# Optimization experiments

Hardware: AMD Instinct MI355X
Metric: run time of the kernel (lower is better)

The kernel has to match this reference:

```python
import jax, jax.numpy as jnp
import numpy as np

D = 1024
H = 16
DH = D // H  # 64


def setup_inputs() -> dict:
    key = jax.random.key(0)
    ks = jax.random.split(key, 11)
    B, S = 2, 2048
    s = 1.0 / np.sqrt(D)  # torch Linear default init scale (uniform bound)
    mk = lambda k, shape: jax.random.uniform(k, shape, jnp.float32, -s, s)
    return {
        "q": jax.random.normal(ks[0], (B, S, D), jnp.float32),
        "k": jax.random.normal(ks[1], (B, S, D), jnp.float32),
        "v": jax.random.normal(ks[2], (B, S, D), jnp.float32),
        "Wq": mk(ks[3], (D, D)), "bq": mk(ks[4], (D,)),
        "Wk": mk(ks[5], (D, D)), "bk": mk(ks[6], (D,)),
        "Wv": mk(ks[7], (D, D)), "bv": mk(ks[8], (D,)),
        "Wo": mk(ks[9], (D, D)), "bo": mk(ks[10], (D,)),
    }


def reference(q, k, v, Wq, bq, Wk, bk, Wv, bv, Wo, bo):
    B, S, _ = q.shape
    scaling = DH ** (-0.5)
    # torch Linear: x @ W.T + b ; then split heads -> (B, H, S, DH)
    split = lambda x: x.reshape(B, -1, H, DH).transpose(0, 2, 1, 3)
    Q = split(q @ Wq.T + bq)
    K = split(k @ Wk.T + bk)
    V = split(v @ Wv.T + bv)
    scores = jnp.einsum("bhqd,bhkd->bhqk", Q, K) * scaling  # [B,H,S,S]
    attn = jax.nn.softmax(scores, axis=-1)
    out = jnp.einsum("bhqk,bhkd->bhqd", attn, V)
    out = out.transpose(0, 2, 1, 3).reshape(B, S, D)
    return out @ Wo.T + bo
```

## Files before the change

kernel.cpp:

```cpp
#include <hip/hip_runtime.h>
#include <stdint.h>

#define DIM   1024
#define HEADS 16
#define DHEAD 64
#define SEQ   2048
#define MROWS 4096
#define NQ    (MROWS * DIM)
#define NW    (DIM * DIM)

typedef unsigned short u16;
typedef __attribute__((ext_vector_type(8))) short short8;
typedef __attribute__((ext_vector_type(4))) float f32x4;
typedef __attribute__((ext_vector_type(16))) float f32x16;

static_assert(sizeof(short8) == 16, "short8 must be 16B");

__device__ __forceinline__ float bf2f(u16 u) {
  union { float f; uint32_t u; } x; x.u = ((uint32_t)u) << 16; return x.f;
}
__device__ __forceinline__ u16 f2bf(float f) {
  union { float f; uint32_t u; } x; x.f = f;
  uint32_t r = x.u + 0x7FFFu + ((x.u >> 16) & 1u);
  return (u16)(r >> 16);
}
__device__ __forceinline__ float asf(uint32_t u) {
  union { float f; uint32_t u; } x; x.u = u; return x.f;
}
__device__ __forceinline__ uint32_t cvtpk(float lo, float hi) {
  uint32_t r;
  asm("v_cvt_pk_bf16_f32 %0, %1, %2" : "=v"(r) : "v"(lo), "v"(hi));
  return r;
}
__device__ __forceinline__ float exp2fast(float x) {
#if __has_builtin(__builtin_amdgcn_exp2f)
  return __builtin_amdgcn_exp2f(x);
#else
  return __expf(x * 0.69314718055994531f);
#endif
}

#if __has_builtin(__builtin_amdgcn_global_load_lds)
#define HAVE_GLLDS 1
#else
#define HAVE_GLLDS 0
#endif

__device__ __forceinline__ void stage16(const u16* src, u16* ldsbase, int cb, int lane) {
#if HAVE_GLLDS
  (void)lane;
  __builtin_amdgcn_global_load_lds((const __attribute__((address_space(1))) void*)src,
                                   (__attribute__((address_space(3))) void*)(ldsbase + (size_t)cb * 8),
                                   16, 0, 0);
#else
  *(short8*)(ldsbase + ((size_t)cb + lane) * 8) = *(const short8*)src;
#endif
}

__global__ __launch_bounds__(256)
void cvt_all(const float* __restrict__ q, const float* __restrict__ k, const float* __restrict__ v,
             const float* __restrict__ wq, const float* __restrict__ wk,
             const float* __restrict__ wv, const float* __restrict__ wo,
             u16* __restrict__ qc, u16* __restrict__ kc, u16* __restrict__ vc,
             u16* __restrict__ wqc, u16* __restrict__ wkc, u16* __restrict__ wvc, u16* __restrict__ woc)
{
  const float* s; u16* d; int n;
  switch (blockIdx.y) {
    case 0: s = q;  d = qc;  n = NQ; break;
    case 1: s = k;  d = kc;  n = NQ; break;
    case 2: s = v;  d = vc;  n = NQ; break;
    case 3: s = wq; d = wqc; n = NW; break;
    case 4: s = wk; d = wkc; n = NW; break;
    case 5: s = wv; d = wvc; n = NW; break;
    default: s = wo; d = woc; n = NW; break;
  }
  const int n8 = n >> 3;
  for (int i = blockIdx.x * blockDim.x + threadIdx.x; i < n8; i += gridDim.x * blockDim.x) {
    float4 f0 = ((const float4*)s)[2 * i];
    float4 f1 = ((const float4*)s)[2 * i + 1];
    union { uint32_t w[4]; short8 s8; } u;
    u.w[0] = cvtpk(f0.x, f0.y); u.w[1] = cvtpk(f0.z, f0.w);
    u.w[2] = cvtpk(f1.x, f1.y); u.w[3] = cvtpk(f1.z, f1.w);
    ((short8*)d)[i] = u.s8;
  }
}

__global__ __launch_bounds__(256)
void gemm_qkv(const u16* __restrict__ A0, const u16* __restrict__ W0, const float* __restrict__ b0, u16* __restrict__ O0, float s0_,
              const u16* __restrict__ A1, const u16* __restrict__ W1, const float* __restrict__ b1, u16* __restrict__ O1, float s1_,
              const u16* __restrict__ A2, const u16* __restrict__ W2, const float* __restrict__ b2, u16* __restrict__ O2, float s2_)
{
  constexpr int BM = 128, BN = 128, BK = 64, RM = 4, RN = 4;
  __shared__ u16 As[BM * BK];
  __shared__ u16 Bs[BN * BK];

  const u16* A = A0; const u16* W = W0; const float* bias = b0; u16* O = O0; float oscale = s0_;
  if (blockIdx.z == 1) { A = A1; W = W1; bias = b1; O = O1; oscale = s1_; }
  else if (blockIdx.z == 2) { A = A2; W = W2; bias = b2; O = O2; oscale = s2_; }

  const int tid  = threadIdx.x;
  const int wave = tid >> 6, lane = tid & 63;
  const int g = lane >> 4, cc = lane & 15;
  const int wr = wave >> 1, wc = wave & 1;
  const int m0 = blockIdx.x * BM, n0 = blockIdx.y * BN;

  f32x4 acc[RM][RN];
  for (int m = 0; m < RM; ++m)
    for (int n = 0; n < RN; ++n) acc[m][n] = (f32x4){0.f, 0.f, 0.f, 0.f};

  for (int k0 = 0; k0 < DIM; k0 += BK) {
    __syncthreads();
    constexpr int AI = (BM * 8) / 256;
    for (int i = 0; i < AI; ++i) {
      int cb = (wave * AI + i) * 64;
      int ch = cb + lane;
      int row = ch >> 3, kc = ch & 7;
      stage16(A + (size_t)(m0 + row) * DIM + k0 + kc * 8, As, cb, lane);
    }
    constexpr int BI = (BN * 8) / 256;
    for (int i = 0; i < BI; ++i) {
      int cb = (wave * BI + i) * 64;
      int ch = cb + lane;
      int row = ch >> 3, kc = ch & 7;
      stage16(W + (size_t)(n0 + row) * DIM + k0 + kc * 8, Bs, cb, lane);
    }
    __syncthreads();

    for (int kk = 0; kk < 2; ++kk) {
      short8 af[RM], bfr[RN];
      for (int m = 0; m < RM; ++m)
        af[m] = *(const short8*)(As + (size_t)(wr * 64 + m * 16 + cc) * BK + kk * 32 + g * 8);
      for (int n = 0; n < RN; ++n)
        bfr[n] = *(const short8*)(Bs + (size_t)(wc * 64 + n * 16 + cc) * BK + kk * 32 + g * 8);
      for (int m = 0; m < RM; ++m)
        for (int n = 0; n < RN; ++n)
          acc[m][n] = __builtin_amdgcn_mfma_f32_16x16x32_bf16(af[m], bfr[n], acc[m][n], 0, 0, 0);
    }
  }

  for (int n = 0; n < RN; ++n) {
    int col = n0 + wc * 64 + n * 16 + cc;
    float bv = bias[col];
    for (int m = 0; m < RM; ++m) {
      int rowb = m0 + wr * 64 + m * 16 + g * 4;
      for (int r = 0; r < 4; ++r) {
        int row = rowb + r;
        float val = (acc[m][n][r] + bv) * oscale;
        int b = row >> 11, s = row & (SEQ - 1);
        int hh = col >> 6, dh = col & 63;
        O[((((size_t)b * HEADS + hh) * SEQ + s) << 6) + dh] = f2bf(val);
      }
    }
  }
}

__global__ __launch_bounds__(256)
void gemm_out(const u16* __restrict__ Op0, const u16* __restrict__ Op1,
              const float* __restrict__ lstats, const u16* __restrict__ W,
              const float* __restrict__ bias, float* __restrict__ Out)
{
  constexpr int BM = 64, BN = 128, BK = 64, RM = 2, RN = 4;
  __shared__ u16 As[BM * BK];
  __shared__ u16 Bs[BN * BK];
  __shared__ float wtab[HEADS * BM];

  const int tid  = threadIdx.x;
  const int wave = tid >> 6, lane = tid & 63;
  const int g = lane >> 4, cc = lane & 15;
  const int wr = wave >> 1, wc = wave & 1;
  const int m0 = blockIdx.x * BM, n0 = blockIdx.y * BN;

  for (int e = tid; e < HEADS * BM; e += 256) {
    int h = e >> 6, r = e & 63;
    int row = m0 + r;
    int b = row >> 11, s = row & (SEQ - 1);
    float l0 = lstats[(size_t)(b * 16 + h) * SEQ + s];
    float l1 = lstats[(size_t)(32 + b * 16 + h) * SEQ + s];
    wtab[e] = 1.0f / (l0 + l1);
  }

  f32x4 acc[RM][RN];
  for (int m = 0; m < RM; ++m)
    for (int n = 0; n < RN; ++n) acc[m][n] = (f32x4){0.f, 0.f, 0.f, 0.f};

  for (int k0 = 0; k0 < DIM; k0 += BK) {
    __syncthreads();
    const int h = k0 >> 6;
    constexpr int AI = (BM * 8) / 256;
    #pragma unroll
    for (int i = 0; i < AI; ++i) {
      int ch = (wave * AI + i) * 64 + lane;
      int row = ch >> 3, kc = ch & 7;
      int grow = m0 + row;
      int b = grow >> 11, s = grow & (SEQ - 1);
      size_t off = ((size_t)(b * 16 + h) * SEQ + s) * 64 + kc * 8;
      short8 a8 = *(const short8*)(Op0 + off);
      short8 b8 = *(const short8*)(Op1 + off);
      float winv = wtab[h * BM + row];
      union { uint32_t w[4]; short8 s8; } u;
      const uint32_t* wa = (const uint32_t*)&a8;
      const uint32_t* wb = (const uint32_t*)&b8;
      #pragma unroll
      for (int j = 0; j < 4; ++j) {
        float lo = (asf(wa[j] << 16) + asf(wb[j] << 16)) * winv;
        float hi2 = (asf(wa[j] & 0xffff0000u) + asf(wb[j] & 0xffff0000u)) * winv;
        u.w[j] = cvtpk(lo, hi2);
      }
      *(short8*)(As + (size_t)ch * 8) = u.s8;
    }
    constexpr int BI = (BN * 8) / 256;
    for (int i = 0; i < BI; ++i) {
      int cb = (wave * BI + i) * 64;
      int ch = cb + lane;
      int row = ch >> 3, kc = ch & 7;
      stage16(W + (size_t)(n0 + row) * DIM + k0 + kc * 8, Bs, cb, lane);
    }
    __syncthreads();

    for (int kk = 0; kk < 2; ++kk) {
      short8 af[RM], bfr[RN];
      for (int m = 0; m < RM; ++m)
        af[m] = *(const short8*)(As + (size_t)(wr * 32 + m * 16 + cc) * BK + kk * 32 + g * 8);
      for (int n = 0; n < RN; ++n)
        bfr[n] = *(const short8*)(Bs + (size_t)(wc * 64 + n * 16 + cc) * BK + kk * 32 + g * 8);
      for (int m = 0; m < RM; ++m)
        for (int n = 0; n < RN; ++n)
          acc[m][n] = __builtin_amdgcn_mfma_f32_16x16x32_bf16(af[m], bfr[n], acc[m][n], 0, 0, 0);
    }
  }

  for (int n = 0; n < RN; ++n) {
    int col = n0 + wc * 64 + n * 16 + cc;
    float bv = bias[col];
    for (int m = 0; m < RM; ++m) {
      int rowb = m0 + wr * 32 + m * 16 + g * 4;
      for (int r = 0; r < 4; ++r)
        Out[(size_t)(rowb + r) * DIM + col] = acc[m][n][r] + bv;
    }
  }
}

#if __has_builtin(__builtin_amdgcn_permlane32_swap)
typedef __attribute__((ext_vector_type(2))) unsigned uint2v;
#define REPACK(PF, A_, B_, C_, D_)                                             \
  {                                                                            \
    uint2v w02 = __builtin_amdgcn_permlane32_swap((A_), (C_), false, false);   \
    uint2v w13 = __builtin_amdgcn_permlane32_swap((B_), (D_), false, false);   \
    union { uint32_t w[4]; short8 s8; } u_;                                    \
    u_.w[0] = w02[0]; u_.w[1] = w13[0]; u_.w[2] = w02[1]; u_.w[3] = w13[1];    \
    PF = u_.s8;                                                                \
  }
#else
#define REPACK(PF, A_, B_, C_, D_)                                             \
  {                                                                            \
    uint32_t pa = __shfl_xor((int)(A_), 32), pb = __shfl_xor((int)(B_), 32);   \
    uint32_t pc = __shfl_xor((int)(C_), 32), pd = __shfl_xor((int)(D_), 32);   \
    union { uint32_t w[4]; short8 s8; } u_;                                    \
    u_.w[0] = hi ? pc : (A_); u_.w[1] = hi ? pd : (B_);                        \
    u_.w[2] = hi ? (C_) : pa; u_.w[3] = hi ? (D_) : pb;                        \
    PF = u_.s8;                                                                \
  }
#endif

#define PV_BLOCK(SS, KSB)                                                      \
  {                                                                            \
    uint32_t a  = cvtpk(SS[0], SS[1]),   b3 = cvtpk(SS[2], SS[3]);             \
    uint32_t c  = cvtpk(SS[4], SS[5]),   d  = cvtpk(SS[6], SS[7]);             \
    uint32_t e  = cvtpk(SS[8], SS[9]),   f  = cvtpk(SS[10], SS[11]);           \
    uint32_t g2 = cvtpk(SS[12], SS[13]), h2 = cvtpk(SS[14], SS[15]);           \
    short8 pf0, pf1;                                                           \
    REPACK(pf0, a, b3, c, d)                                                   \
    REPACK(pf1, e, f, g2, h2)                                                  \
    uint32_t kvb0 = (uint32_t)((KSB) * 64 + hi * 16), kvb1 = kvb0 + 32;        \
    uint32_t r0 = (uint32_t)l31, r1 = 32u + (uint32_t)l31;                     \
    uint32_t sw = ((uint32_t)l31 & 7) << 4;                                    \
    short8 vf00 = *(const short8*)(Vc + ((r0 * 128 + kvb0) ^ sw));             \
    short8 vf01 = *(const short8*)(Vc + ((r1 * 128 + kvb0) ^ sw));             \
    short8 vf10 = *(const short8*)(Vc + ((r0 * 128 + kvb1) ^ sw));             \
    short8 vf11 = *(const short8*)(Vc + ((r1 * 128 + kvb1) ^ sw));             \
    __builtin_amdgcn_s_setprio(1);                                             \
    o0 = __builtin_amdgcn_mfma_f32_32x32x16_bf16(vf00, pf0, o0, 0, 0, 0);      \
    o1 = __builtin_amdgcn_mfma_f32_32x32x16_bf16(vf01, pf0, o1, 0, 0, 0);      \
    o0 = __builtin_amdgcn_mfma_f32_32x32x16_bf16(vf10, pf1, o0, 0, 0, 0);      \
    o1 = __builtin_amdgcn_mfma_f32_32x32x16_bf16(vf11, pf1, o1, 0, 0, 0);      \
    __builtin_amdgcn_s_setprio(0);                                             \
  }

__global__ __launch_bounds__(256)
void attn_fwd6(const u16* __restrict__ Qb, const u16* __restrict__ Kb,
               const u16* __restrict__ Vb, u16* __restrict__ Opart,
               float* __restrict__ lstats)
{
  uint32_t lid = blockIdx.x;
  uint32_t logical = (lid & 7) * 128 + (lid >> 3);
  const int qt    = logical & 15;
  const int bh    = (logical >> 4) & 31;
  const int split = logical >> 9;

  const int q0 = qt * 128;
  const int kvbase = split * (SEQ / 2);
  const int tid = threadIdx.x, wave = tid >> 6, lane = tid & 63;
  const int l31 = lane & 31, hi = lane >> 5;
  const float MFIX = 20.0f;

  const size_t base = (size_t)bh * SEQ * DHEAD;
  const u16* Qg = Qb + base;
  const u16* Kg = Kb + base;
  const u16* Vg = Vb + base;

  __shared__ u16 Ks[2][64 * 64];
  __shared__ u16 Vts[2][64 * 64];

  short8 qf[4];
  {
    const u16* qrow = Qg + (size_t)(q0 + wave * 32 + l31) * DHEAD + hi * 8;
    for (int ks = 0; ks < 4; ++ks)
      qf[ks] = *(const short8*)(qrow + ks * 16);
  }

  f32x16 o0, o1;
  for (int r = 0; r < 16; ++r) { o0[r] = 0.f; o1[r] = 0.f; }
  float l = 0.f;

  const int rp = tid & 31, c8 = tid >> 5;
  const int kr = tid >> 3, kc0 = tid & 7;
  short8 ka, kb2, va, vb2;

  {
    const int kv0 = kvbase;
    ka  = *(const short8*)(Kg + (size_t)(kv0 + kr) * DHEAD + kc0 * 8);
    kb2 = *(const short8*)(Kg + (size_t)(kv0 + 32 + kr) * DHEAD + kc0 * 8);
    va  = *(const short8*)(Vg + (size_t)(kv0 + 2 * rp) * DHEAD + c8 * 8);
    vb2 = *(const short8*)(Vg + (size_t)(kv0 + 2 * rp + 1) * DHEAD + c8 * 8);
    uint32_t sw = ((uint32_t)kr & 7) << 4;
    *(short8*)((char*)Ks[0] + (((uint32_t)kr * 128 + (uint32_t)kc0 * 16) ^ sw)) = ka;
    *(short8*)((char*)Ks[0] + ((((uint32_t)kr + 32) * 128 + (uint32_t)kc0 * 16) ^ sw)) = kb2;
    for (int j = 0; j < 8; ++j) {
      uint32_t row = c8 * 8 + j;
      uint32_t byte = (row * 128 + rp * 4) ^ ((row & 7) << 4);
      *(uint32_t*)((char*)Vts[0] + byte) =
          (uint32_t)(u16)va[j] | ((uint32_t)(u16)vb2[j] << 16);
    }
  }
  __syncthreads();

  for (int t = 0; t < 16; ++t) {
    const int cur = t & 1;
    if (t < 15) {
      const int kv0 = kvbase + (t + 1) * 64;
      ka  = *(const short8*)(Kg + (size_t)(kv0 + kr) * DHEAD + kc0 * 8);
      kb2 = *(const short8*)(Kg + (size_t)(kv0 + 32 + kr) * DHEAD + kc0 * 8);
      va  = *(const short8*)(Vg + (size_t)(kv0 + 2 * rp) * DHEAD + c8 * 8);
      vb2 = *(const short8*)(Vg + (size_t)(kv0 + 2 * rp + 1) * DHEAD + c8 * 8);
    }

    const char* Kc = (const char*)Ks[cur];
    const char* Vc = (const char*)Vts[cur];

    f32x16 s0, s1;
    for (int r = 0; r < 16; ++r) { s0[r] = -MFIX; s1[r] = -MFIX; }
    {
      uint32_t rb0 = (uint32_t)l31 * 128, sw0 = ((uint32_t)l31 & 7) << 4;
      uint32_t cbyte = (uint32_t)hi * 16;
      short8 k0 = *(const short8*)(Kc + ((rb0 + cbyte     ) ^ sw0));
      short8 k1 = *(const short8*)(Kc + ((rb0 + cbyte + 32) ^ sw0));
      short8 k2 = *(const short8*)(Kc + ((rb0 + cbyte + 64) ^ sw0));
      short8 k3 = *(const short8*)(Kc + ((rb0 + cbyte + 96) ^ sw0));
      uint32_t rb1 = rb0 + 32 * 128;
      short8 k4 = *(const short8*)(Kc + ((rb1 + cbyte     ) ^ sw0));
      short8 k5 = *(const short8*)(Kc + ((rb1 + cbyte + 32) ^ sw0));
      short8 k6 = *(const short8*)(Kc + ((rb1 + cbyte + 64) ^ sw0));
      short8 k7 = *(const short8*)(Kc + ((rb1 + cbyte + 96) ^ sw0));
      __builtin_amdgcn_s_setprio(1);
      s0 = __builtin_amdgcn_mfma_f32_32x32x16_bf16(k0, qf[0], s0, 0, 0, 0);
      s0 = __builtin_amdgcn_mfma_f32_32x32x16_bf16(k1, qf[1], s0, 0, 0, 0);
      s0 = __builtin_amdgcn_mfma_f32_32x32x16_bf16(k2, qf[2], s0, 0, 0, 0);
      s0 = __builtin_amdgcn_mfma_f32_32x32x16_bf16(k3, qf[3], s0, 0, 0, 0);
      s1 = __builtin_amdgcn_mfma_f32_32x32x16_bf16(k4, qf[0], s1, 0, 0, 0);
      s1 = __builtin_amdgcn_mfma_f32_32x32x16_bf16(k5, qf[1], s1, 0, 0, 0);
      s1 = __builtin_amdgcn_mfma_f32_32x32x16_bf16(k6, qf[2], s1, 0, 0, 0);
      s1 = __builtin_amdgcn_mfma_f32_32x32x16_bf16(k7, qf[3], s1, 0, 0, 0);
      __builtin_amdgcn_s_setprio(0);
    }

    for (int r = 0; r < 16; ++r) s0[r] = exp2fast(s0[r]);
    for (int r = 0; r < 16; ++r) s1[r] = exp2fast(s1[r]);
    {
      float a0 = s0[0] + s1[0], a1 = s0[1] + s1[1];
      float a2 = s0[2] + s1[2], a3 = s0[3] + s1[3];
      for (int r = 4; r < 16; r += 4) {
        a0 += s0[r]     + s1[r];
        a1 += s0[r + 1] + s1[r + 1];
        a2 += s0[r + 2] + s1[r + 2];
        a3 += s0[r + 3] + s1[r + 3];
      }
      float rsum = (a0 + a1) + (a2 + a3);
      rsum += __shfl_xor(rsum, 32);
      l += rsum;
    }

    PV_BLOCK(s0, 0)
    PV_BLOCK(s1, 1)

    if (t < 15) {
      uint32_t sw = ((uint32_t)kr & 7) << 4;
      char* Kn = (char*)Ks[cur ^ 1];
      *(short8*)(Kn + (((uint32_t)kr * 128 + (uint32_t)kc0 * 16) ^ sw)) = ka;
      *(short8*)(Kn + ((((uint32_t)kr + 32) * 128 + (uint32_t)kc0 * 16) ^ sw)) = kb2;
      char* Vn = (char*)Vts[cur ^ 1];
      for (int j = 0; j < 8; ++j) {
        uint32_t row = c8 * 8 + j;
        uint32_t byte = (row * 128 + rp * 4) ^ ((row & 7) << 4);
        *(uint32_t*)(Vn + byte) =
            (uint32_t)(u16)va[j] | ((uint32_t)(u16)vb2[j] << 16);
      }
      __syncthreads();
    }
  }

  const int q = q0 + wave * 32 + l31;
  u16* orow = Opart + (((size_t)split * 32 + bh) * SEQ + q) * DHEAD;
  for (int db = 0; db < 2; ++db) {
    const f32x16& o = db ? o1 : o0;
    for (int gq = 0; gq < 4; ++gq) {
      int dh = db * 32 + gq * 8 + hi * 4;
      ushort4 w;
      w.x = f2bf(o[gq * 4 + 0]); w.y = f2bf(o[gq * 4 + 1]);
      w.z = f2bf(o[gq * 4 + 2]); w.w = f2bf(o[gq * 4 + 3]);
      *(ushort4*)(orow + dh) = w;
    }
  }
  if (hi == 0)
    lstats[((size_t)split * 32 + bh) * SEQ + q] = l;
}

extern "C" void kernel_launch(void* const* d_in, const int* in_sizes, int n_in,
                              void* d_out, int out_size, void* d_ws, size_t ws_size,
                              hipStream_t stream)
{
  const float* q  = (const float*)d_in[0];
  const float* k  = (const float*)d_in[1];
  const float* v  = (const float*)d_in[2];
  const float* Wq = (const float*)d_in[3];
  const float* bq = (const float*)d_in[4];
  const float* Wk = (const float*)d_in[5];
  const float* bk = (const float*)d_in[6];
  const float* Wv = (const float*)d_in[7];
  const float* bv = (const float*)d_in[8];
  const float* Wo = (const float*)d_in[9];
  const float* bo = (const float*)d_in[10];
  float* out = (float*)d_out;

  u16* qc  = (u16*)d_ws;
  u16* kc  = qc  + NQ;
  u16* vc  = kc  + NQ;
  u16* wqc = vc  + NQ;
  u16* wkc = wqc + NW;
  u16* wvc = wkc + NW;
  u16* woc = wvc + NW;
  u16* Qh  = woc + NW;
  u16* Kh  = Qh  + NQ;
  u16* Vh  = Kh  + NQ;

  u16* Op0 = (u16*)d_ws;
  u16* Op1 = Op0 + NQ;
  float* lstats = (float*)(Op1 + NQ);

  dim3 blk(256);
  hipLaunchKernelGGL(cvt_all, dim3(512, 7, 1), blk, 0, stream,
                     q, k, v, Wq, Wk, Wv, Wo, qc, kc, vc, wqc, wkc, wvc, woc);
  hipLaunchKernelGGL(gemm_qkv, dim3(MROWS / 128, DIM / 128, 3), blk, 0, stream,
                     qc, wqc, bq, Qh, 0.125f * 1.4426950408889634f,
                     kc, wkc, bk, Kh, 1.0f,
                     vc, wvc, bv, Vh, 1.0f);
  hipLaunchKernelGGL(attn_fwd6, dim3(1024, 1, 1), blk, 0, stream, Qh, Kh, Vh, Op0, lstats);
  hipLaunchKernelGGL(gemm_out, dim3(MROWS / 64, DIM / 128, 1), blk, 0, stream,
                     Op0, Op1, lstats, woc, bo, out);
}
```

Baseline: 143.1 us.

## Switch projection GEMMs to 32x32 MFMA with XOR-swizzled LDS and block remap

Both the QKV projection and output projection GEMMs now use 32x32x16 bf16 MFMA tiles instead of 16x16x32. Shared-memory tiles are stored with an XOR swizzle on the 16-byte column chunk to avoid bank conflicts. Block indices are remapped to improve L2 locality, and s_setprio brackets the MFMA bursts. The aim is fewer LDS reads per FLOP and better matrix-core utilisation. The cost is more complex epilogue indexing and higher accumulator register pressure.

```diff
diff --git a/kernel.cpp b/kernel.cpp
--- a/kernel.cpp
+++ b/kernel.cpp
@@ -11,7 +11,6 @@
 
 typedef unsigned short u16;
 typedef __attribute__((ext_vector_type(8))) short short8;
-typedef __attribute__((ext_vector_type(4))) float f32x4;
 typedef __attribute__((ext_vector_type(16))) float f32x16;
 
 static_assert(sizeof(short8) == 16, "short8 must be 16B");
@@ -90,7 +89,7 @@
               const u16* __restrict__ A1, const u16* __restrict__ W1, const float* __restrict__ b1, u16* __restrict__ O1, float s1_,
               const u16* __restrict__ A2, const u16* __restrict__ W2, const float* __restrict__ b2, u16* __restrict__ O2, float s2_)
 {
-  constexpr int BM = 128, BN = 128, BK = 64, RM = 4, RN = 4;
+  constexpr int BM = 128, BN = 128, BK = 64;
   __shared__ u16 As[BM * BK];
   __shared__ u16 Bs[BN * BK];
 
@@ -100,13 +99,15 @@
 
   const int tid  = threadIdx.x;
   const int wave = tid >> 6, lane = tid & 63;
-  const int g = lane >> 4, cc = lane & 15;
+  const int l31 = lane & 31, hi = lane >> 5;
   const int wr = wave >> 1, wc = wave & 1;
-  const int m0 = blockIdx.x * BM, n0 = blockIdx.y * BN;
-
-  f32x4 acc[RM][RN];
-  for (int m = 0; m < RM; ++m)
-    for (int n = 0; n < RN; ++n) acc[m][n] = (f32x4){0.f, 0.f, 0.f, 0.f};
+  const int bx = ((blockIdx.x & 7) << 2) | (blockIdx.x >> 3);
+  const int m0 = bx * BM, n0 = blockIdx.y * BN;
+
+  f32x16 acc[2][2];
+  for (int mb = 0; mb < 2; ++mb)
+    for (int nb = 0; nb < 2; ++nb)
+      for (int r = 0; r < 16; ++r) acc[mb][nb][r] = 0.f;
 
   for (int k0 = 0; k0 < DIM; k0 += BK) {
     __syncthreads();
@@ -115,39 +116,52 @@
       int cb = (wave * AI + i) * 64;
       int ch = cb + lane;
       int row = ch >> 3, kc = ch & 7;
-      stage16(A + (size_t)(m0 + row) * DIM + k0 + kc * 8, As, cb, lane);
+      stage16(A + (size_t)(m0 + row) * DIM + k0 + (kc ^ (row & 7)) * 8, As, cb, lane);
     }
     constexpr int BI = (BN * 8) / 256;
     for (int i = 0; i < BI; ++i) {
       int cb = (wave * BI + i) * 64;
       int ch = cb + lane;
       int row = ch >> 3, kc = ch & 7;
-      stage16(W + (size_t)(n0 + row) * DIM + k0 + kc * 8, Bs, cb, lane);
+      stage16(W + (size_t)(n0 + row) * DIM + k0 + (kc ^ (row & 7)) * 8, Bs, cb, lane);
     }
     __syncthreads();
 
-    for (int kk = 0; kk < 2; ++kk) {
-      short8 af[RM], bfr[RN];
-      for (int m = 0; m < RM; ++m)
-        af[m] = *(const short8*)(As + (size_t)(wr * 64 + m * 16 + cc) * BK + kk * 32 + g * 8);
-      for (int n = 0; n < RN; ++n)
-        bfr[n] = *(const short8*)(Bs + (size_t)(wc * 64 + n * 16 + cc) * BK + kk * 32 + g * 8);
-      for (int m = 0; m < RM; ++m)
-        for (int n = 0; n < RN; ++n)
-          acc[m][n] = __builtin_amdgcn_mfma_f32_16x16x32_bf16(af[m], bfr[n], acc[m][n], 0, 0, 0);
-    }
-  }
-
-  for (int n = 0; n < RN; ++n) {
-    int col = n0 + wc * 64 + n * 16 + cc;
+    #pragma unroll
+    for (int kk = 0; kk < 4; ++kk) {
+      short8 af[2], bf[2];
+      #pragma unroll
+      for (int mb = 0; mb < 2; ++mb) {
+        uint32_t row = (uint32_t)(wr * 64 + mb * 32 + l31);
+        af[mb] = *(const short8*)((const char*)As +
+                   (row * 128 + ((uint32_t)(kk * 32 + hi * 16) ^ ((row & 7) << 4))));
+      }
+      #pragma unroll
+      for (int nb = 0; nb < 2; ++nb) {
+        uint32_t row = (uint32_t)(wc * 64 + nb * 32 + l31);
+        bf[nb] = *(const short8*)((const char*)Bs +
+                   (row * 128 + ((uint32_t)(kk * 32 + hi * 16) ^ ((row & 7) << 4))));
+      }
+      __builtin_amdgcn_s_setprio(1);
+      #pragma unroll
+      for (int mb = 0; mb < 2; ++mb)
+        #pragma unroll
+        for (int nb = 0; nb < 2; ++nb)
+          acc[mb][nb] = __builtin_amdgcn_mfma_f32_32x32x16_bf16(af[mb], bf[nb], acc[mb][nb], 0, 0, 0);
+      __builtin_amdgcn_s_setprio(0);
+    }
+  }
+
+  for (int nb = 0; nb < 2; ++nb) {
+    int col = n0 + wc * 64 + nb * 32 + l31;
     float bv = bias[col];
-    for (int m = 0; m < RM; ++m) {
-      int rowb = m0 + wr * 64 + m * 16 + g * 4;
-      for (int r = 0; r < 4; ++r) {
-        int row = rowb + r;
-        float val = (acc[m][n][r] + bv) * oscale;
+    int hh = col >> 6, dh = col & 63;
+    for (int mb = 0; mb < 2; ++mb) {
+      int rowb = m0 + wr * 64 + mb * 32 + hi * 4;
+      for (int r = 0; r < 16; ++r) {
+        int row = rowb + (r & 3) + ((r >> 2) << 3);
+        float val = (acc[mb][nb][r] + bv) * oscale;
         int b = row >> 11, s = row & (SEQ - 1);
-        int hh = col >> 6, dh = col & 63;
         O[((((size_t)b * HEADS + hh) * SEQ + s) << 6) + dh] = f2bf(val);
       }
     }
@@ -159,16 +173,17 @@
               const float* __restrict__ lstats, const u16* __restrict__ W,
               const float* __restrict__ bias, float* __restrict__ Out)
 {
-  constexpr int BM = 64, BN = 128, BK = 64, RM = 2, RN = 4;
+  constexpr int BM = 64, BN = 128, BK = 64;
   __shared__ u16 As[BM * BK];
   __shared__ u16 Bs[BN * BK];
   __shared__ float wtab[HEADS * BM];
 
   const int tid  = threadIdx.x;
   const int wave = tid >> 6, lane = tid & 63;
-  const int g = lane >> 4, cc = lane & 15;
+  const int l31 = lane & 31, hi = lane >> 5;
   const int wr = wave >> 1, wc = wave & 1;
-  const int m0 = blockIdx.x * BM, n0 = blockIdx.y * BN;
+  const int bx = ((blockIdx.x & 7) << 3) | (blockIdx.x >> 3);
+  const int m0 = bx * BM, n0 = blockIdx.y * BN;
 
   for (int e = tid; e < HEADS * BM; e += 256) {
     int h = e >> 6, r = e & 63;
@@ -179,9 +194,9 @@
     wtab[e] = 1.0f / (l0 + l1);
   }
 
-  f32x4 acc[RM][RN];
-  for (int m = 0; m < RM; ++m)
-    for (int n = 0; n < RN; ++n) acc[m][n] = (f32x4){0.f, 0.f, 0.f, 0.f};
+  f32x16 acc[2];
+  for (int nb = 0; nb < 2; ++nb)
+    for (int r = 0; r < 16; ++r) acc[nb][r] = 0.f;
 
   for (int k0 = 0; k0 < DIM; k0 += BK) {
     __syncthreads();
@@ -206,36 +221,46 @@
         float hi2 = (asf(wa[j] & 0xffff0000u) + asf(wb[j] & 0xffff0000u)) * winv;
         u.w[j] = cvtpk(lo, hi2);
       }
-      *(short8*)(As + (size_t)ch * 8) = u.s8;
+      *(short8*)((char*)As + (((uint32_t)row * 128 + (uint32_t)kc * 16) ^ (((uint32_t)row & 7) << 4))) = u.s8;
     }
     constexpr int BI = (BN * 8) / 256;
     for (int i = 0; i < BI; ++i) {
       int cb = (wave * BI + i) * 64;
       int ch = cb + lane;
       int row = ch >> 3, kc = ch & 7;
-      stage16(W + (size_t)(n0 + row) * DIM + k0 + kc * 8, Bs, cb, lane);
+      stage16(W + (size_t)(n0 + row) * DIM + k0 + (kc ^ (row & 7)) * 8, Bs, cb, lane);
     }
     __syncthreads();
 
-    for (int kk = 0; kk < 2; ++kk) {
-      short8 af[RM], bfr[RN];
-      for (int m = 0; m < RM; ++m)
-        af[m] = *(const short8*)(As + (size_t)(wr * 32 + m * 16 + cc) * BK + kk * 32 + g * 8);
-      for (int n = 0; n < RN; ++n)
-        bfr[n] = *(const short8*)(Bs + (size_t)(wc * 64 + n * 16 + cc) * BK + kk * 32 + g * 8);
-      for (int m = 0; m < RM; ++m)
-        for (int n = 0; n < RN; ++n)
-          acc[m][n] = __builtin_amdgcn_mfma_f32_16x16x32_bf16(af[m], bfr[n], acc[m][n], 0, 0, 0);
-    }
-  }
-
-  for (int n = 0; n < RN; ++n) {
-    int col = n0 + wc * 64 + n * 16 + cc;
+    #pragma unroll
+    for (int kk = 0; kk < 4; ++kk) {
+      short8 af, bf[2];
+      {
+        uint32_t row = (uint32_t)(wr * 32 + l31);
+        af = *(const short8*)((const char*)As +
+               (row * 128 + ((uint32_t)(kk * 32 + hi * 16) ^ ((row & 7) << 4))));
+      }
+      #pragma unroll
+      for (int nb = 0; nb < 2; ++nb) {
+        uint32_t row = (uint32_t)(wc * 64 + nb * 32 + l31);
+        bf[nb] = *(const short8*)((const char*)Bs +
+                   (row * 128 + ((uint32_t)(kk * 32 + hi * 16) ^ ((row & 7) << 4))));
+      }
+      __builtin_amdgcn_s_setprio(1);
+      #pragma unroll
+      for (int nb = 0; nb < 2; ++nb)
+        acc[nb] = __builtin_amdgcn_mfma_f32_32x32x16_bf16(af, bf[nb], acc[nb], 0, 0, 0);
+      __builtin_amdgcn_s_setprio(0);
+    }
+  }
+
+  for (int nb = 0; nb < 2; ++nb) {
+    int col = n0 + wc * 64 + nb * 32 + l31;
     float bv = bias[col];
-    for (int m = 0; m < RM; ++m) {
-      int rowb = m0 + wr * 32 + m * 16 + g * 4;
-      for (int r = 0; r < 4; ++r)
-        Out[(size_t)(rowb + r) * DIM + col] = acc[m][n][r] + bv;
+    int rowb = m0 + wr * 32 + hi * 4;
+    for (int r = 0; r < 16; ++r) {
+      int row = rowb + (r & 3) + ((r >> 2) << 3);
+      Out[(size_t)row * DIM + col] = acc[nb][r] + bv;
     }
   }
 }
```

Result: faster. 124.6 us (-12.9%).
